# Kernel optimization log

Hardware: AMD Instinct MI355X
Metric: run time of the kernel (lower is better)

The kernel has to match this reference:

```python
import jax, jax.numpy as jnp
import numpy as np

B = 64          # number of samples / segments
LATENT = 256    # RSSM latent dim
N = 4_000_000   # total points
TEMPERATURE = 1.0


def setup_inputs() -> dict:
    key = jax.random.key(0)
    k1, k2, k3, k4 = jax.random.split(key, 4)
    coherence_spatial = jax.random.normal(k1, (N,), dtype=jnp.float32)
    posterior_mean = jax.random.normal(k2, (B, LATENT), dtype=jnp.float32)
    # std must be positive; uniform in [0.5, 1.5)
    posterior_std = jax.random.uniform(k3, (B, LATENT), dtype=jnp.float32, minval=0.5, maxval=1.5)
    batch = jax.random.randint(k4, (N,), 0, B, dtype=jnp.int64)
    return {
        'coherence_spatial': coherence_spatial,
        'posterior_mean': posterior_mean,
        'posterior_std': posterior_std,
        'batch': batch,
    }


def reference(coherence_spatial, posterior_mean, posterior_std, batch):
    # uncertainty: Gaussian entropy per dim, summed over latent -> (B,)
    two_pi_e = 2.0 * jnp.pi * jnp.e
    entropy = 0.5 * jnp.log(two_pi_e * jnp.square(posterior_std))  # (B, LATENT)
    uncertainty = entropy.sum(axis=-1)                              # (B,)

    # priority_i = coherence_i * uncertainty[batch_i]
    priority = coherence_spatial * uncertainty[batch]               # (N,)

    # fused segment-softmax over ragged segments defined by `batch`
    logits = priority / TEMPERATURE
    seg_max = jax.ops.segment_max(logits, batch, num_segments=B)    # (B,)
    e = jnp.exp(logits - seg_max[batch])                            # (N,)
    seg_sum = jax.ops.segment_sum(e, batch, num_segments=B)         # (B,)
    priority_normalized = e / seg_sum[batch]                        # (N,)

    return priority, priority_normalized, uncertainty
```

## Files before the change

### kernel.cpp

```cpp
#include <hip/hip_runtime.h>

#define BSEG   64
#define LATENT 256
#define NB     2048
#define ITERS  2
#define SCALE_F   2097152.0f
#define INV_SCALE 4.76837158203125e-7
#define ENC_NEG_INF 0x007FFFFFu

typedef float vfloat4 __attribute__((ext_vector_type(4)));
typedef int   vint4   __attribute__((ext_vector_type(4)));
typedef unsigned vuint4 __attribute__((ext_vector_type(4)));

__device__ __forceinline__ unsigned enc_bits(unsigned u) {
    return (u & 0x80000000u) ? ~u : (u | 0x80000000u);
}
__device__ __forceinline__ float dec_f32(unsigned e) {
    unsigned u = (e & 0x80000000u) ? (e & 0x7FFFFFFFu) : ~e;
    return __uint_as_float(u);
}

__global__ __launch_bounds__(256) void k_unc(const float* __restrict__ pstd,
                                             float* __restrict__ unc,
                                             float* __restrict__ out_unc) {
    int b = blockIdx.x;
    float v = __logf(pstd[b * LATENT + threadIdx.x]);
#pragma unroll
    for (int off = 32; off > 0; off >>= 1) v += __shfl_down(v, off, 64);
    __shared__ float part[4];
    int lane = threadIdx.x & 63, wv = threadIdx.x >> 6;
    if (lane == 0) part[wv] = v;
    __syncthreads();
    if (threadIdx.x == 0) {
        float s = part[0] + part[1] + part[2] + part[3];
        float u = 128.0f * 2.83787706640934548f + s;
        unc[b]     = u;
        out_unc[b] = u;
    }
}

__global__ __launch_bounds__(256, 8) void k_pass1(
    const float* __restrict__ coh, const int* __restrict__ batch,
    const float* __restrict__ unc,
    float* __restrict__ bmax_t,
    float* __restrict__ bsum_t,
    float* __restrict__ pri, int n) {
    __shared__ float    unc_s[BSEG];
    __shared__ unsigned max_s[4][BSEG];
    __shared__ unsigned sum_s[4][BSEG];
    __shared__ float    m_s[BSEG];

    int t = threadIdx.x, wv = t >> 6;
    if (t < BSEG) {
        unc_s[t] = unc[t];
#pragma unroll
        for (int w = 0; w < 4; ++w) { max_s[w][t] = ENC_NEG_INF; sum_s[w][t] = 0u; }
    }
    __syncthreads();

    int gid = blockIdx.x * 256 + t;
    int nv  = n >> 2;

    vuint4 pw[ITERS];
#pragma unroll
    for (int u = 0; u < ITERS; ++u) {
        int i = gid + u * (NB * 256);
        if (i < nv) {
            vfloat4 cv = __builtin_nontemporal_load((const vfloat4*)coh + i);
            vint4   bv = __builtin_nontemporal_load((const vint4*)batch + i);
            vuint4 w;
            w.x = (__float_as_uint(cv.x * unc_s[bv.x]) & ~63u) | (unsigned)bv.x;
            w.y = (__float_as_uint(cv.y * unc_s[bv.y]) & ~63u) | (unsigned)bv.y;
            w.z = (__float_as_uint(cv.z * unc_s[bv.z]) & ~63u) | (unsigned)bv.z;
            w.w = (__float_as_uint(cv.w * unc_s[bv.w]) & ~63u) | (unsigned)bv.w;
            ((vuint4*)pri)[i] = w;
            pw[u] = w;
            atomicMax(&max_s[wv][bv.x], enc_bits(w.x & ~63u));
            atomicMax(&max_s[wv][bv.y], enc_bits(w.y & ~63u));
            atomicMax(&max_s[wv][bv.z], enc_bits(w.z & ~63u));
            atomicMax(&max_s[wv][bv.w], enc_bits(w.w & ~63u));
        }
    }
    unsigned w_t = 0u; int b_t = -1;
    if (blockIdx.x == 0) {
        int rem = n - (nv << 2);
        if (t < rem) {
            int i = (nv << 2) + t;
            b_t = batch[i];
            float p = coh[i] * unc_s[b_t];
            w_t = (__float_as_uint(p) & ~63u) | (unsigned)b_t;
            ((unsigned*)pri)[i] = w_t;
            atomicMax(&max_s[wv][b_t], enc_bits(w_t & ~63u));
        }
    }
    __syncthreads();
    if (t < BSEG) {
        unsigned m = max(max(max_s[0][t], max_s[1][t]), max(max_s[2][t], max_s[3][t]));
        float mf = dec_f32(m);
        m_s[t] = mf;
        bmax_t[t * NB + blockIdx.x] = mf;
    }
    __syncthreads();

#pragma unroll
    for (int u = 0; u < ITERS; ++u) {
        int i = gid + u * (NB * 256);
        if (i < nv) {
            vuint4 w = pw[u];
            int s0 = w.x & 63, s1 = w.y & 63, s2 = w.z & 63, s3 = w.w & 63;
            atomicAdd(&sum_s[wv][s0], (unsigned)(__expf(__uint_as_float(w.x & ~63u) - m_s[s0]) * SCALE_F));
            atomicAdd(&sum_s[wv][s1], (unsigned)(__expf(__uint_as_float(w.y & ~63u) - m_s[s1]) * SCALE_F));
            atomicAdd(&sum_s[wv][s2], (unsigned)(__expf(__uint_as_float(w.z & ~63u) - m_s[s2]) * SCALE_F));
            atomicAdd(&sum_s[wv][s3], (unsigned)(__expf(__uint_as_float(w.w & ~63u) - m_s[s3]) * SCALE_F));
        }
    }
    if (b_t >= 0)
        atomicAdd(&sum_s[wv][b_t], (unsigned)(__expf(__uint_as_float(w_t & ~63u) - m_s[b_t]) * SCALE_F));
    __syncthreads();
    if (t < BSEG) {
        unsigned long long tot = (unsigned long long)sum_s[0][t] + sum_s[1][t]
                               + (unsigned long long)sum_s[2][t] + sum_s[3][t];
        bsum_t[t * NB + blockIdx.x] = (float)((double)tot * INV_SCALE);
    }
}

__global__ __launch_bounds__(256) void k_combine(const float* __restrict__ bmax_t,
                                                 const float* __restrict__ bsum_t,
                                                 float* __restrict__ maxf,
                                                 float* __restrict__ rsum) {
    int s = blockIdx.x, t = threadIdx.x;
    const float* bm = bmax_t + s * NB;
    const float* bs = bsum_t + s * NB;
    float m = -INFINITY;
    for (int i = t; i < NB; i += 256) m = fmaxf(m, __builtin_nontemporal_load(bm + i));
#pragma unroll
    for (int off = 32; off > 0; off >>= 1) m = fmaxf(m, __shfl_down(m, off, 64));
    __shared__ float part[4];
    if ((t & 63) == 0) part[t >> 6] = m;
    __syncthreads();
    float m_g = fmaxf(fmaxf(part[0], part[1]), fmaxf(part[2], part[3]));
    double acc = 0.0;
    for (int i = t; i < NB; i += 256) {
        float bmi = bm[i];
        float d = bmi - m_g;
        if (d < -100.0f) d = -100.0f;
        acc += (double)__builtin_nontemporal_load(bs + i) * (double)expf(d);
    }
#pragma unroll
    for (int off = 32; off > 0; off >>= 1) acc += __shfl_down(acc, off, 64);
    __shared__ double part2[4];
    if ((t & 63) == 0) part2[t >> 6] = acc;
    __syncthreads();
    if (t == 0) {
        double tot = part2[0] + part2[1] + part2[2] + part2[3];
        maxf[s] = m_g;
        rsum[s] = (tot > 0.0) ? (float)(1.0 / tot) : 0.0f;
    }
}

__global__ __launch_bounds__(256, 8) void k_pass2(
    const float* __restrict__ pri,
    const float* __restrict__ maxf, const float* __restrict__ rsum,
    float* __restrict__ nrm, int n) {
    __shared__ float m_s[BSEG];
    __shared__ float r_s[BSEG];
    int t = threadIdx.x;
    if (t < BSEG) { m_s[t] = maxf[t]; r_s[t] = rsum[t]; }
    __syncthreads();
    int gid = blockIdx.x * 256 + t;
    int gstride = NB * 256;
    int nv = n >> 2;
    for (int i = gid; i < nv; i += gstride) {
        vuint4 w = ((const vuint4*)pri)[i];
        int s0 = w.x & 63, s1 = w.y & 63, s2 = w.z & 63, s3 = w.w & 63;
        vfloat4 ov;
        ov.x = __expf(__uint_as_float(w.x & ~63u) - m_s[s0]) * r_s[s0];
        ov.y = __expf(__uint_as_float(w.y & ~63u) - m_s[s1]) * r_s[s1];
        ov.z = __expf(__uint_as_float(w.z & ~63u) - m_s[s2]) * r_s[s2];
        ov.w = __expf(__uint_as_float(w.w & ~63u) - m_s[s3]) * r_s[s3];
        __builtin_nontemporal_store(ov, (vfloat4*)nrm + i);
    }
    for (int i = (nv << 2) + gid; i < n; i += gstride) {
        unsigned w = ((const unsigned*)pri)[i];
        int b = w & 63;
        nrm[i] = __expf(__uint_as_float(w & ~63u) - m_s[b]) * r_s[b];
    }
}

extern "C" void kernel_launch(void* const* d_in, const int* in_sizes, int n_in,
                              void* d_out, int out_size, void* d_ws, size_t ws_size,
                              hipStream_t stream) {
    const float* coh   = (const float*)d_in[0];
    const float* pstd  = (const float*)d_in[2];
    const int*   batch = (const int*)d_in[3];
    int n = in_sizes[0];

    float* out     = (float*)d_out;
    float* out_pri = out;
    float* out_nrm = out + n;
    float* out_unc = out + 2 * (size_t)n;

    size_t part_bytes = (size_t)NB * BSEG * 4;
    float* ws_unc  = (float*)d_ws;
    float* ws_maxf = (float*)((char*)d_ws + 256);
    float* ws_rsum = (float*)((char*)d_ws + 512);
    float* ws_bmax = (float*)((char*)d_ws + 1024);
    float* ws_bsum = (float*)((char*)d_ws + 1024 + part_bytes);

    k_unc    <<<BSEG, 256, 0, stream>>>(pstd, ws_unc, out_unc);
    k_pass1  <<<NB,   256, 0, stream>>>(coh, batch, ws_unc, ws_bmax, ws_bsum,
                                        out_pri, n);
    k_combine<<<BSEG, 256, 0, stream>>>(ws_bmax, ws_bsum, ws_maxf, ws_rsum);
    k_pass2  <<<NB,   256, 0, stream>>>(out_pri, ws_maxf, ws_rsum, out_nrm, n);
}
```

Before: 34.32 us.

## Fold combine kernel into pass1 via last-block ticket and halve pass1 grid

Removes the separate combine kernel: each pass1 block takes a ticket from a global atomic counter, and the last block to finish reduces all per-block max/sum partials into the per-segment max and reciprocal sum. Pass1 now runs 1024 blocks doing 4 iterations each, with partials stored block-major and plain loads in place of nontemporal loads. This saves one kernel launch and halves the partial buffers, but the final reduction now runs serially on a single block while the other blocks sit idle. The ticket counter is never reset; it relies on a modulo check and on the workspace starting at zero.

```diff
diff --git a/kernel.cpp b/kernel.cpp
--- a/kernel.cpp
+++ b/kernel.cpp
@@ -2,14 +2,14 @@
 
 #define BSEG   64
 #define LATENT 256
-#define NB     2048
-#define ITERS  2
+#define NB1    1024
+#define ITERS  4
+#define NB2    2048
 #define SCALE_F   2097152.0f
 #define INV_SCALE 4.76837158203125e-7
 #define ENC_NEG_INF 0x007FFFFFu
 
 typedef float vfloat4 __attribute__((ext_vector_type(4)));
-typedef int   vint4   __attribute__((ext_vector_type(4)));
 typedef unsigned vuint4 __attribute__((ext_vector_type(4)));
 
 __device__ __forceinline__ unsigned enc_bits(unsigned u) {
@@ -42,8 +42,10 @@
 __global__ __launch_bounds__(256, 8) void k_pass1(
     const float* __restrict__ coh, const int* __restrict__ batch,
     const float* __restrict__ unc,
-    float* __restrict__ bmax_t,
-    float* __restrict__ bsum_t,
+    float* __restrict__ bmax,
+    float* __restrict__ bsum,
+    float* __restrict__ maxf, float* __restrict__ rsum,
+    unsigned* __restrict__ ticket,
     float* __restrict__ pri, int n) {
     __shared__ float    unc_s[BSEG];
     __shared__ unsigned max_s[4][BSEG];
@@ -64,10 +66,10 @@
     vuint4 pw[ITERS];
 #pragma unroll
     for (int u = 0; u < ITERS; ++u) {
-        int i = gid + u * (NB * 256);
+        int i = gid + u * (NB1 * 256);
         if (i < nv) {
-            vfloat4 cv = __builtin_nontemporal_load((const vfloat4*)coh + i);
-            vint4   bv = __builtin_nontemporal_load((const vint4*)batch + i);
+            float4 cv = ((const float4*)coh)[i];
+            int4   bv = ((const int4*)batch)[i];
             vuint4 w;
             w.x = (__float_as_uint(cv.x * unc_s[bv.x]) & ~63u) | (unsigned)bv.x;
             w.y = (__float_as_uint(cv.y * unc_s[bv.y]) & ~63u) | (unsigned)bv.y;
@@ -79,6 +81,8 @@
             atomicMax(&max_s[wv][bv.y], enc_bits(w.y & ~63u));
             atomicMax(&max_s[wv][bv.z], enc_bits(w.z & ~63u));
             atomicMax(&max_s[wv][bv.w], enc_bits(w.w & ~63u));
+        } else {
+            pw[u].x = 0xFFFFFFFFu;
         }
     }
     unsigned w_t = 0u; int b_t = -1;
@@ -98,15 +102,14 @@
         unsigned m = max(max(max_s[0][t], max_s[1][t]), max(max_s[2][t], max_s[3][t]));
         float mf = dec_f32(m);
         m_s[t] = mf;
-        bmax_t[t * NB + blockIdx.x] = mf;
+        bmax[blockIdx.x * BSEG + t] = mf;
     }
     __syncthreads();
 
 #pragma unroll
     for (int u = 0; u < ITERS; ++u) {
-        int i = gid + u * (NB * 256);
-        if (i < nv) {
-            vuint4 w = pw[u];
+        vuint4 w = pw[u];
+        if (w.x != 0xFFFFFFFFu) {
             int s0 = w.x & 63, s1 = w.y & 63, s2 = w.z & 63, s3 = w.w & 63;
             atomicAdd(&sum_s[wv][s0], (unsigned)(__expf(__uint_as_float(w.x & ~63u) - m_s[s0]) * SCALE_F));
             atomicAdd(&sum_s[wv][s1], (unsigned)(__expf(__uint_as_float(w.y & ~63u) - m_s[s1]) * SCALE_F));
@@ -120,41 +123,41 @@
     if (t < BSEG) {
         unsigned long long tot = (unsigned long long)sum_s[0][t] + sum_s[1][t]
                                + (unsigned long long)sum_s[2][t] + sum_s[3][t];
-        bsum_t[t * NB + blockIdx.x] = (float)((double)tot * INV_SCALE);
-    }
-}
-
-__global__ __launch_bounds__(256) void k_combine(const float* __restrict__ bmax_t,
-                                                 const float* __restrict__ bsum_t,
-                                                 float* __restrict__ maxf,
-                                                 float* __restrict__ rsum) {
-    int s = blockIdx.x, t = threadIdx.x;
-    const float* bm = bmax_t + s * NB;
-    const float* bs = bsum_t + s * NB;
+        bsum[blockIdx.x * BSEG + t] = (float)((double)tot * INV_SCALE);
+    }
+
+    __shared__ int last_flag;
+    if (t == 0) {
+        __threadfence();
+        unsigned old = atomicAdd(ticket, 1u);
+        last_flag = ((old & (NB1 - 1u)) == (NB1 - 1u));
+    }
+    __syncthreads();
+    if (!last_flag) return;
+    __threadfence();
+
+    int s = t & 63, q = t >> 6;
+    const int CH = NB1 / 4;
     float m = -INFINITY;
-    for (int i = t; i < NB; i += 256) m = fmaxf(m, __builtin_nontemporal_load(bm + i));
-#pragma unroll
-    for (int off = 32; off > 0; off >>= 1) m = fmaxf(m, __shfl_down(m, off, 64));
-    __shared__ float part[4];
-    if ((t & 63) == 0) part[t >> 6] = m;
-    __syncthreads();
-    float m_g = fmaxf(fmaxf(part[0], part[1]), fmaxf(part[2], part[3]));
+    for (int r = q * CH; r < (q + 1) * CH; ++r)
+        m = fmaxf(m, bmax[r * BSEG + s]);
+    __shared__ float mq[4][BSEG];
+    mq[q][s] = m;
+    __syncthreads();
+    float m_g = fmaxf(fmaxf(mq[0][s], mq[1][s]), fmaxf(mq[2][s], mq[3][s]));
     double acc = 0.0;
-    for (int i = t; i < NB; i += 256) {
-        float bmi = bm[i];
-        float d = bmi - m_g;
+    for (int r = q * CH; r < (q + 1) * CH; ++r) {
+        float d = bmax[r * BSEG + s] - m_g;
         if (d < -100.0f) d = -100.0f;
-        acc += (double)__builtin_nontemporal_load(bs + i) * (double)expf(d);
-    }
-#pragma unroll
-    for (int off = 32; off > 0; off >>= 1) acc += __shfl_down(acc, off, 64);
-    __shared__ double part2[4];
-    if ((t & 63) == 0) part2[t >> 6] = acc;
-    __syncthreads();
-    if (t == 0) {
-        double tot = part2[0] + part2[1] + part2[2] + part2[3];
-        maxf[s] = m_g;
-        rsum[s] = (tot > 0.0) ? (float)(1.0 / tot) : 0.0f;
+        acc += (double)bsum[r * BSEG + s] * (double)__expf(d);
+    }
+    __shared__ double aq[4][BSEG];
+    aq[q][s] = acc;
+    __syncthreads();
+    if (t < BSEG) {
+        double tot = aq[0][t] + aq[1][t] + aq[2][t] + aq[3][t];
+        maxf[t] = fmaxf(fmaxf(mq[0][t], mq[1][t]), fmaxf(mq[2][t], mq[3][t]));
+        rsum[t] = (tot > 0.0) ? (float)(1.0 / tot) : 0.0f;
     }
 }
 
@@ -168,7 +171,7 @@
     if (t < BSEG) { m_s[t] = maxf[t]; r_s[t] = rsum[t]; }
     __syncthreads();
     int gid = blockIdx.x * 256 + t;
-    int gstride = NB * 256;
+    int gstride = NB2 * 256;
     int nv = n >> 2;
     for (int i = gid; i < nv; i += gstride) {
         vuint4 w = ((const vuint4*)pri)[i];
@@ -200,16 +203,16 @@
     float* out_nrm = out + n;
     float* out_unc = out + 2 * (size_t)n;
 
-    size_t part_bytes = (size_t)NB * BSEG * 4;
-    float* ws_unc  = (float*)d_ws;
-    float* ws_maxf = (float*)((char*)d_ws + 256);
-    float* ws_rsum = (float*)((char*)d_ws + 512);
-    float* ws_bmax = (float*)((char*)d_ws + 1024);
-    float* ws_bsum = (float*)((char*)d_ws + 1024 + part_bytes);
-
-    k_unc    <<<BSEG, 256, 0, stream>>>(pstd, ws_unc, out_unc);
-    k_pass1  <<<NB,   256, 0, stream>>>(coh, batch, ws_unc, ws_bmax, ws_bsum,
-                                        out_pri, n);
-    k_combine<<<BSEG, 256, 0, stream>>>(ws_bmax, ws_bsum, ws_maxf, ws_rsum);
-    k_pass2  <<<NB,   256, 0, stream>>>(out_pri, ws_maxf, ws_rsum, out_nrm, n);
-}
+    size_t part_bytes = (size_t)NB1 * BSEG * 4;
+    float*    ws_unc    = (float*)d_ws;
+    float*    ws_maxf   = (float*)((char*)d_ws + 256);
+    float*    ws_rsum   = (float*)((char*)d_ws + 512);
+    unsigned* ws_ticket = (unsigned*)((char*)d_ws + 768);
+    float*    ws_bmax   = (float*)((char*)d_ws + 1024);
+    float*    ws_bsum   = (float*)((char*)d_ws + 1024 + part_bytes);
+
+    k_unc  <<<BSEG, 256, 0, stream>>>(pstd, ws_unc, out_unc);
+    k_pass1<<<NB1,  256, 0, stream>>>(coh, batch, ws_unc, ws_bmax, ws_bsum,
+                                      ws_maxf, ws_rsum, ws_ticket, out_pri, n);
+    k_pass2<<<NB2,  256, 0, stream>>>(out_pri, ws_maxf, ws_rsum, out_nrm, n);
+}
```

After: 94.68 us. 176% more time.
